# Optimization experiments

Hardware: AMD Instinct MI355X
Metric: run time of the kernel (lower is better)

Reference implementation:

```python
import jax, jax.numpy as jnp
import numpy as np

DECAY = 0.8
COMMITMENT_WEIGHT = 1.0
EPS = 1e-5


def setup_inputs() -> dict:
    key = jax.random.key(0)
    k1, k2, k3 = jax.random.split(key, 3)
    B, T, D, K = 16, 2048, 512, 8192
    x = jax.random.normal(k1, (B, T, D), dtype=jnp.float32)
    embed = jax.random.normal(k2, (D, K), dtype=jnp.float32)
    cluster_size = jnp.ones((K,), dtype=jnp.float32)
    embed_avg = jax.random.normal(k3, (D, K), dtype=jnp.float32)
    return {"x": x, "embed": embed, "cluster_size": cluster_size, "embed_avg": embed_avg}


def reference(x, embed, cluster_size, embed_avg):
    B, T, D = x.shape
    K = embed.shape[1]
    flat = x.reshape(-1, D)  # [N, D]

    # squared L2 distance to each code: ||f||^2 - 2 f.e + ||e||^2  -> [N, K]
    dist = (flat * flat).sum(-1, keepdims=True) \
        - 2.0 * (flat @ embed) \
        + (embed * embed).sum(0, keepdims=True)
    embed_ind = jnp.argmin(dist, axis=1)  # [N] (== argmax of -dist)

    quantize = jnp.take(embed.T, embed_ind, axis=0).reshape(B, T, D)

    # ---- EMA codebook statistics (training-mode buffer updates) ----
    onehot_sum = jnp.zeros((K,), dtype=flat.dtype).at[embed_ind].add(1.0)  # [K]
    # flat.T @ onehot == segment-sum of tokens per code, transposed -> [D, K]
    embed_sum = jax.ops.segment_sum(flat, embed_ind, num_segments=K).T
    new_cluster_size = cluster_size * DECAY + (1.0 - DECAY) * onehot_sum
    new_embed_avg = embed_avg * DECAY + (1.0 - DECAY) * embed_sum
    n = new_cluster_size.sum()
    cs = (new_cluster_size + EPS) / (n + K * EPS) * n
    new_embed = new_embed_avg / cs[None, :]
    # (random re-init of unused codes is omitted: non-deterministic side effect)

    commitment_loss = jnp.mean((jax.lax.stop_gradient(quantize) - x) ** 2) * COMMITMENT_WEIGHT
    quantize_st = x + jax.lax.stop_gradient(quantize - x)  # straight-through

    return (quantize_st, embed_ind.reshape(B, T), commitment_loss,
            new_embed, new_cluster_size, new_embed_avg)
```

## Files before the change

### kernel.cpp

```cpp
#include <hip/hip_runtime.h>

#define NTOK   32768
#define DDIM   512
#define KCODES 8192
#define DK     (DDIM * KCODES)
#define DECAYF 0.8f
#define EPSF   1e-5f

using short8 = __attribute__((ext_vector_type(8))) short;
using f32x4  = __attribute__((ext_vector_type(4))) float;

#define WS_ESUMT  0
#define WS_ONEHOT DK
#define WS_ENORM  (DK + 8192)
#define WS_SCAL   (DK + 16384)
#define WS_PART   (WS_SCAL + 64)
#define WS_EHI    (WS_PART + 2 * NTOK)
#define WS_ELO    (WS_EHI + DK / 2)

__device__ __forceinline__ unsigned short bf16rne(float f) {
  unsigned u = __float_as_uint(f);
  unsigned r = u + 0x7FFFu + ((u >> 16) & 1u);
  return (unsigned short)(r >> 16);
}

__device__ __forceinline__ void gload_lds16(const unsigned short* g, unsigned short* l) {
  __builtin_amdgcn_global_load_lds(
      (const __attribute__((address_space(1))) unsigned int*)g,
      (__attribute__((address_space(3))) unsigned int*)l, 16, 0, 0);
}

__global__ __launch_bounds__(256) void prep_kernel(
    const float* __restrict__ x, const float* __restrict__ embed,
    const float* __restrict__ cluster_size,
    unsigned short* __restrict__ xhi, unsigned short* __restrict__ xlo,
    unsigned short* __restrict__ ehi, unsigned short* __restrict__ elo,
    float* __restrict__ e_norm, float* __restrict__ esumT,
    float* __restrict__ onehot, float* __restrict__ scal,
    unsigned long long* __restrict__ partials) {
  __shared__ float tile[32][33];
  __shared__ float part[8][32];
  __shared__ float w[4];
  const int bid = blockIdx.x;
  const int tid = threadIdx.x;

  if (bid < 8192) {
    const size_t i = ((size_t)bid * 256 + tid) * 8;
    const float4 v0 = *(const float4*)&x[i];
    const float4 v1 = *(const float4*)&x[i + 4];
    const float v[8] = {v0.x, v0.y, v0.z, v0.w, v1.x, v1.y, v1.z, v1.w};
    unsigned short h[8], l[8];
#pragma unroll
    for (int j = 0; j < 8; ++j) {
      h[j] = bf16rne(v[j]);
      l[j] = bf16rne(v[j] - __uint_as_float((unsigned)h[j] << 16));
    }
    uint4 H, L;
    H.x = h[0] | ((unsigned)h[1] << 16); H.y = h[2] | ((unsigned)h[3] << 16);
    H.z = h[4] | ((unsigned)h[5] << 16); H.w = h[6] | ((unsigned)h[7] << 16);
    L.x = l[0] | ((unsigned)l[1] << 16); L.y = l[2] | ((unsigned)l[3] << 16);
    L.z = l[4] | ((unsigned)l[5] << 16); L.w = l[6] | ((unsigned)l[7] << 16);
    *(uint4*)&xhi[i] = H;
    *(uint4*)&xlo[i] = L;
  } else if (bid < 8192 + 256) {
    const int k0 = (bid - 8192) * 32;
    const int tx = tid & 31;
    const int ty = tid >> 5;
    float sq = 0.f;
#pragma unroll 1
    for (int d0 = 0; d0 < DDIM; d0 += 32) {
      __syncthreads();
#pragma unroll
      for (int j = 0; j < 4; ++j) {
        const int dl = ty + j * 8;
        const float v = embed[(size_t)(d0 + dl) * KCODES + k0 + tx];
        tile[dl][tx] = v;
        sq += v * v;
      }
      __syncthreads();
#pragma unroll
      for (int j = 0; j < 4; ++j) {
        const int kl = ty + j * 8;
        const size_t idx = (size_t)(k0 + kl) * DDIM + d0 + tx;
        const float v = tile[tx][kl];
        const unsigned short h = bf16rne(v);
        ehi[idx] = h;
        elo[idx] = bf16rne(v - __uint_as_float((unsigned)h << 16));
      }
    }
    part[ty][tx] = sq;
    __syncthreads();
    if (ty == 0) {
      float s = 0.f;
#pragma unroll
      for (int j = 0; j < 8; ++j) s += part[j][tx];
      e_norm[k0 + tx] = s;
    }
  } else if (bid < 8192 + 256 + 2048) {
    const int zb = bid - (8192 + 256);
    const size_t off = (size_t)zb * 2048 + (size_t)tid * 8;
    const float4 z = {0.f, 0.f, 0.f, 0.f};
    *(float4*)&esumT[off] = z;
    *(float4*)&esumT[off + 4] = z;
  } else {
    const int b = bid - (8192 + 256 + 2048);
    onehot[b * 256 + tid] = 0.f;
    const size_t pbase = (size_t)b * 1024 + (size_t)tid * 4;
    const ulonglong2 ff = {~0ull, ~0ull};
    *(ulonglong2*)&partials[pbase] = ff;
    *(ulonglong2*)&partials[pbase + 2] = ff;
    float s = cluster_size[b * 256 + tid];
#pragma unroll
    for (int off = 32; off > 0; off >>= 1) s += __shfl_down(s, off);
    if ((tid & 63) == 0) w[tid >> 6] = s;
    __syncthreads();
    if (tid == 0) {
      scal[2 + b] = w[0] + w[1] + w[2] + w[3];
      if (b == 0) { scal[0] = 0.f; scal[1] = 0.f; }
    }
  }
}

__global__ __launch_bounds__(256) void argmin_mfma_kernel(
    const unsigned short* __restrict__ xhi, const unsigned short* __restrict__ xlo,
    const unsigned short* __restrict__ ehi, const unsigned short* __restrict__ elo,
    const float* __restrict__ e_norm, unsigned long long* __restrict__ partials) {
  __shared__ unsigned short Ahs[128 * 32];
  __shared__ unsigned short Als[128 * 32];
  __shared__ unsigned short Bhs[128 * 32];
  __shared__ unsigned short Bls[128 * 32];

  const int t    = threadIdx.x;
  const int wid  = t >> 6;
  const int lid  = t & 63;
  const int kblk = blockIdx.x;
  const int tokbase = blockIdx.y * 128;
  const int kbase   = kblk * 128;

  const int wrow = wid >> 1, wcol = wid & 1;
  const int m16  = lid & 15, kq = lid >> 4;

  const int srow = lid >> 2;
  const int gcol = ((lid & 3) ^ ((srow >> 1) & 3)) * 8;
  const int fsw = (kq ^ ((m16 >> 1) & 3)) * 8;

  f32x4 acc[4][4];
#pragma unroll
  for (int i = 0; i < 4; ++i)
#pragma unroll
    for (int j = 0; j < 4; ++j) acc[i][j] = (f32x4)0.f;

  const unsigned short* Ahg = xhi + (size_t)tokbase * DDIM;
  const unsigned short* Alg = xlo + (size_t)tokbase * DDIM;
  const unsigned short* Bhg = ehi + (size_t)kbase * DDIM;
  const unsigned short* Blg = elo + (size_t)kbase * DDIM;

#pragma unroll 1
  for (int d0 = 0; d0 < DDIM; d0 += 32) {
    __syncthreads();
#pragma unroll
    for (int p = 0; p < 2; ++p) {
      const int chunk = wid + p * 4;
      const size_t go = (size_t)(chunk * 16 + srow) * DDIM + d0 + gcol;
      gload_lds16(Ahg + go, &Ahs[chunk * 512]);
      gload_lds16(Alg + go, &Als[chunk * 512]);
      gload_lds16(Bhg + go, &Bhs[chunk * 512]);
      gload_lds16(Blg + go, &Bls[chunk * 512]);
    }
    __syncthreads();
    short8 bh[4], bl[4];
#pragma unroll
    for (int j = 0; j < 4; ++j) {
      const int r = (wcol * 64 + j * 16 + m16) * 32 + fsw;
      bh[j] = *(const short8*)&Bhs[r];
      bl[j] = *(const short8*)&Bls[r];
    }
#pragma unroll
    for (int i = 0; i < 4; ++i) {
      const int r = (wrow * 64 + i * 16 + m16) * 32 + fsw;
      const short8 ah = *(const short8*)&Ahs[r];
      const short8 al = *(const short8*)&Als[r];
#pragma unroll
      for (int j = 0; j < 4; ++j) {
        acc[i][j] = __builtin_amdgcn_mfma_f32_16x16x32_bf16(ah, bh[j], acc[i][j], 0, 0, 0);
        acc[i][j] = __builtin_amdgcn_mfma_f32_16x16x32_bf16(ah, bl[j], acc[i][j], 0, 0, 0);
        acc[i][j] = __builtin_amdgcn_mfma_f32_16x16x32_bf16(al, bh[j], acc[i][j], 0, 0, 0);
      }
    }
  }

  float en[4];
#pragma unroll
  for (int j = 0; j < 4; ++j)
    en[j] = e_norm[kbase + wcol * 64 + j * 16 + m16];

  __syncthreads();
  unsigned long long* red = (unsigned long long*)Ahs;
#pragma unroll
  for (int i = 0; i < 4; ++i) {
#pragma unroll
    for (int r = 0; r < 4; ++r) {
      unsigned long long best = 0xFFFFFFFFFFFFFFFFull;
#pragma unroll
      for (int j = 0; j < 4; ++j) {
        const float s = en[j] - 2.0f * acc[i][j][r];
        unsigned u = __float_as_uint(s);
        u = (u & 0x80000000u) ? ~u : (u | 0x80000000u);
        const unsigned k = (unsigned)(kbase + wcol * 64 + j * 16 + m16);
        const unsigned long long c = ((unsigned long long)u << 32) | k;
        best = (c < best) ? c : best;
      }
#pragma unroll
      for (int s = 1; s < 16; s <<= 1) {
        const unsigned long long c = __shfl_xor(best, s);
        best = (c < best) ? c : best;
      }
      if (m16 == 0)
        red[(wrow * 64 + i * 16 + kq * 4 + r) * 2 + wcol] = best;
    }
  }
  __syncthreads();
  if (t < 128) {
    const unsigned long long a0 = red[t * 2], a1 = red[t * 2 + 1];
    const unsigned long long m = (a0 < a1) ? a0 : a1;
    atomicMin(&partials[tokbase + t], m);
  }
}

__global__ __launch_bounds__(256) void gather_stats_kernel(
    const float* __restrict__ x, const unsigned short* __restrict__ ehi,
    const unsigned short* __restrict__ elo,
    const unsigned long long* __restrict__ partials,
    float* __restrict__ quant_out, float* __restrict__ indf_out,
    float* __restrict__ embed_sumT, float* __restrict__ onehot,
    float* __restrict__ scal) {
  const int sub = threadIdx.x >> 7;
  const int t7  = threadIdx.x & 127;
  const int n   = blockIdx.x * 2 + sub;
  __shared__ int s_ind[2];
  __shared__ float wsum[4];
  if (t7 == 0) {
    const int k = (int)(partials[n] & 0xFFFFFFFFull);
    s_ind[sub] = k;
    indf_out[n] = (float)k;
    atomicAdd(&onehot[k], 1.0f);
  }
  __syncthreads();
  const int k = s_ind[sub];
  const int d4 = t7 * 4;
  const ushort4 h4 = *(const ushort4*)&ehi[(size_t)k * DDIM + d4];
  const ushort4 l4 = *(const ushort4*)&elo[(size_t)k * DDIM + d4];
  float4 e;
  e.x = __uint_as_float((unsigned)h4.x << 16) + __uint_as_float((unsigned)l4.x << 16);
  e.y = __uint_as_float((unsigned)h4.y << 16) + __uint_as_float((unsigned)l4.y << 16);
  e.z = __uint_as_float((unsigned)h4.z << 16) + __uint_as_float((unsigned)l4.z << 16);
  e.w = __uint_as_float((unsigned)h4.w << 16) + __uint_as_float((unsigned)l4.w << 16);
  const float4 xv = *(const float4*)&x[(size_t)n * DDIM + d4];
  *(float4*)&quant_out[(size_t)n * DDIM + d4] = e;
  atomicAdd(&embed_sumT[(size_t)k * DDIM + d4 + 0], xv.x);
  atomicAdd(&embed_sumT[(size_t)k * DDIM + d4 + 1], xv.y);
  atomicAdd(&embed_sumT[(size_t)k * DDIM + d4 + 2], xv.z);
  atomicAdd(&embed_sumT[(size_t)k * DDIM + d4 + 3], xv.w);
  const float dx0 = e.x - xv.x, dx1 = e.y - xv.y, dx2 = e.z - xv.z, dx3 = e.w - xv.w;
  float ls = dx0 * dx0 + dx1 * dx1 + dx2 * dx2 + dx3 * dx3;
#pragma unroll
  for (int off = 32; off > 0; off >>= 1) ls += __shfl_down(ls, off);
  if ((threadIdx.x & 63) == 0) wsum[threadIdx.x >> 6] = ls;
  __syncthreads();
  if (threadIdx.x == 0)
    atomicAdd(&scal[0], wsum[0] + wsum[1] + wsum[2] + wsum[3]);
}

__global__ __launch_bounds__(256) void finalize_kernel(
    const float* __restrict__ embed_avg, const float* __restrict__ embed_sumT,
    const float* __restrict__ cluster_size, const float* __restrict__ onehot,
    const float* __restrict__ scal,
    float* __restrict__ out_embed, float* __restrict__ out_avg,
    float* __restrict__ out_ncs, float* __restrict__ out_loss) {
  __shared__ float tile[32][33];
  __shared__ float sh_nsum;
  const int k0 = blockIdx.x * 32;
  const int d0 = blockIdx.y * 32;
  const int tx = threadIdx.x & 31;
  const int ty = threadIdx.x >> 5;
  if (threadIdx.x == 0) {
    float s = 0.f;
#pragma unroll
    for (int b = 0; b < 32; ++b) s += scal[2 + b];
    sh_nsum = DECAYF * s + (1.0f - DECAYF) * (float)NTOK;
  }
#pragma unroll
  for (int j = 0; j < 4; ++j) {
    const int kl = ty + j * 8;
    tile[kl][tx] = embed_sumT[(size_t)(k0 + kl) * DDIM + d0 + tx];
  }
  __syncthreads();
  const float nsum = sh_nsum;
  const float ncs = DECAYF * cluster_size[k0 + tx] + (1.0f - DECAYF) * onehot[k0 + tx];
  const float csv = (ncs + EPSF) / (nsum + (float)KCODES * EPSF) * nsum;
#pragma unroll
  for (int j = 0; j < 4; ++j) {
    const int dl = ty + j * 8;
    const size_t idx = (size_t)(d0 + dl) * KCODES + k0 + tx;
    const float nea = DECAYF * embed_avg[idx] + (1.0f - DECAYF) * tile[tx][dl];
    out_avg[idx] = nea;
    out_embed[idx] = nea / csv;
  }
  if (blockIdx.y == 0 && ty == 0)
    out_ncs[k0 + tx] = ncs;
  if (blockIdx.x == 0 && blockIdx.y == 0 && threadIdx.x == 0)
    out_loss[0] = scal[0] * (1.0f / ((float)NTOK * (float)DDIM));
}

extern "C" void kernel_launch(void* const* d_in, const int* in_sizes, int n_in,
                              void* d_out, int out_size, void* d_ws, size_t ws_size,
                              hipStream_t stream) {
  (void)in_sizes; (void)n_in; (void)out_size; (void)ws_size;
  const float* x            = (const float*)d_in[0];
  const float* embed        = (const float*)d_in[1];
  const float* cluster_size = (const float*)d_in[2];
  const float* embed_avg    = (const float*)d_in[3];

  float* out = (float*)d_out;
  float* out_quant = out;
  float* out_indf  = out + 16777216;
  float* out_loss  = out + 16777216 + 32768;
  float* out_embed = out + 16777216 + 32768 + 1;
  float* out_ncs   = out_embed + DK;
  float* out_avg   = out_ncs + KCODES;

  float* ws = (float*)d_ws;
  float* esumT  = ws + WS_ESUMT;
  float* onehot = ws + WS_ONEHOT;
  float* e_norm = ws + WS_ENORM;
  float* scal   = ws + WS_SCAL;
  unsigned long long* partials = (unsigned long long*)(ws + WS_PART);
  unsigned short* ehi = (unsigned short*)(ws + WS_EHI);
  unsigned short* elo = (unsigned short*)(ws + WS_ELO);

  unsigned short* xhi = (unsigned short*)d_out;
  unsigned short* xlo = xhi + (size_t)NTOK * DDIM;

  prep_kernel<<<8192 + 256 + 2048 + 32, 256, 0, stream>>>(
      x, embed, cluster_size, xhi, xlo, ehi, elo, e_norm, esumT, onehot, scal, partials);

  argmin_mfma_kernel<<<dim3(64, 256), 256, 0, stream>>>(
      xhi, xlo, ehi, elo, e_norm, partials);

  gather_stats_kernel<<<NTOK / 2, 256, 0, stream>>>(
      x, ehi, elo, partials, out_quant, out_indf, esumT, onehot, scal);

  finalize_kernel<<<dim3(KCODES / 32, DDIM / 32), 256, 0, stream>>>(
      embed_avg, esumT, cluster_size, onehot, scal,
      out_embed, out_avg, out_ncs, out_loss);
}
```

Measured before the change: 1.382 ms.

## Fuse four VQ kernels into one persistent cooperative kernel with grid syncs

Merges the prep, MFMA argmin, gather/stats and finalize kernels into one persistent cooperative kernel. Work items are distributed in grid-stride loops, and the phases are separated by grid.sync. This removes three kernel launches and the idle gaps between them. In exchange, the grid is capped at occupancy times 256 blocks, grid barriers are added, and the argmin block order changes, which may hurt cache reuse.

```diff
diff --git a/kernel.cpp b/kernel.cpp
--- a/kernel.cpp
+++ b/kernel.cpp
@@ -1,4 +1,7 @@
 #include <hip/hip_runtime.h>
+#include <hip/hip_cooperative_groups.h>
+
+namespace cg = cooperative_groups;
 
 #define NTOK   32768
 #define DDIM   512
@@ -18,6 +21,11 @@
 #define WS_EHI    (WS_PART + 2 * NTOK)
 #define WS_ELO    (WS_EHI + DK / 2)
 
+#define P_NBLK (8192 + 256 + 2048 + 32)
+#define G_NBLK (64 * 256)
+#define Q_NBLK (NTOK / 2)
+#define F_NBLK (256 * 16)
+
 __device__ __forceinline__ unsigned short bf16rne(float f) {
   unsigned u = __float_as_uint(f);
   unsigned r = u + 0x7FFFu + ((u >> 16) & 1u);
@@ -30,286 +38,290 @@
       (__attribute__((address_space(3))) unsigned int*)l, 16, 0, 0);
 }
 
-__global__ __launch_bounds__(256) void prep_kernel(
+__global__ __launch_bounds__(256, 3) void vq_fused_kernel(
     const float* __restrict__ x, const float* __restrict__ embed,
-    const float* __restrict__ cluster_size,
+    const float* __restrict__ cluster_size, const float* __restrict__ embed_avg,
+    float* __restrict__ out_quant, float* __restrict__ out_indf,
+    float* __restrict__ out_loss, float* __restrict__ out_embed,
+    float* __restrict__ out_ncs, float* __restrict__ out_avg,
     unsigned short* __restrict__ xhi, unsigned short* __restrict__ xlo,
     unsigned short* __restrict__ ehi, unsigned short* __restrict__ elo,
     float* __restrict__ e_norm, float* __restrict__ esumT,
     float* __restrict__ onehot, float* __restrict__ scal,
     unsigned long long* __restrict__ partials) {
-  __shared__ float tile[32][33];
-  __shared__ float part[8][32];
-  __shared__ float w[4];
-  const int bid = blockIdx.x;
+  __shared__ __align__(16) unsigned short sbuf[4 * 128 * 32];
+  cg::grid_group grid = cg::this_grid();
   const int tid = threadIdx.x;
-
-  if (bid < 8192) {
-    const size_t i = ((size_t)bid * 256 + tid) * 8;
-    const float4 v0 = *(const float4*)&x[i];
-    const float4 v1 = *(const float4*)&x[i + 4];
-    const float v[8] = {v0.x, v0.y, v0.z, v0.w, v1.x, v1.y, v1.z, v1.w};
-    unsigned short h[8], l[8];
-#pragma unroll
-    for (int j = 0; j < 8; ++j) {
-      h[j] = bf16rne(v[j]);
-      l[j] = bf16rne(v[j] - __uint_as_float((unsigned)h[j] << 16));
+  const int nb  = gridDim.x;
+
+  {
+    float* tile33 = (float*)sbuf;
+    float* part8  = tile33 + 32 * 33;
+    float* wred   = part8 + 8 * 32;
+    for (int bid = blockIdx.x; bid < P_NBLK; bid += nb) {
+      if (bid < 8192) {
+        const size_t i = ((size_t)bid * 256 + tid) * 8;
+        const float4 v0 = *(const float4*)&x[i];
+        const float4 v1 = *(const float4*)&x[i + 4];
+        const float v[8] = {v0.x, v0.y, v0.z, v0.w, v1.x, v1.y, v1.z, v1.w};
+        unsigned short h[8], l[8];
+#pragma unroll
+        for (int j = 0; j < 8; ++j) {
+          h[j] = bf16rne(v[j]);
+          l[j] = bf16rne(v[j] - __uint_as_float((unsigned)h[j] << 16));
+        }
+        uint4 H, L;
+        H.x = h[0] | ((unsigned)h[1] << 16); H.y = h[2] | ((unsigned)h[3] << 16);
+        H.z = h[4] | ((unsigned)h[5] << 16); H.w = h[6] | ((unsigned)h[7] << 16);
+        L.x = l[0] | ((unsigned)l[1] << 16); L.y = l[2] | ((unsigned)l[3] << 16);
+        L.z = l[4] | ((unsigned)l[5] << 16); L.w = l[6] | ((unsigned)l[7] << 16);
+        *(uint4*)&xhi[i] = H;
+        *(uint4*)&xlo[i] = L;
+      } else if (bid < 8192 + 256) {
+        const int k0 = (bid - 8192) * 32;
+        const int tx = tid & 31;
+        const int ty = tid >> 5;
+        float sq = 0.f;
+#pragma unroll 1
+        for (int d0 = 0; d0 < DDIM; d0 += 32) {
+          __syncthreads();
+#pragma unroll
+          for (int j = 0; j < 4; ++j) {
+            const int dl = ty + j * 8;
+            const float v = embed[(size_t)(d0 + dl) * KCODES + k0 + tx];
+            tile33[dl * 33 + tx] = v;
+            sq += v * v;
+          }
+          __syncthreads();
+#pragma unroll
+          for (int j = 0; j < 4; ++j) {
+            const int kl = ty + j * 8;
+            const size_t idx = (size_t)(k0 + kl) * DDIM + d0 + tx;
+            const float v = tile33[tx * 33 + kl];
+            const unsigned short h = bf16rne(v);
+            ehi[idx] = h;
+            elo[idx] = bf16rne(v - __uint_as_float((unsigned)h << 16));
+          }
+        }
+        part8[ty * 32 + tx] = sq;
+        __syncthreads();
+        if (ty == 0) {
+          float s = 0.f;
+#pragma unroll
+          for (int j = 0; j < 8; ++j) s += part8[j * 32 + tx];
+          e_norm[k0 + tx] = s;
+        }
+      } else if (bid < 8192 + 256 + 2048) {
+        const int zb = bid - (8192 + 256);
+        const size_t off = (size_t)zb * 2048 + (size_t)tid * 8;
+        const float4 z = {0.f, 0.f, 0.f, 0.f};
+        *(float4*)&esumT[off] = z;
+        *(float4*)&esumT[off + 4] = z;
+      } else {
+        const int b = bid - (8192 + 256 + 2048);
+        onehot[b * 256 + tid] = 0.f;
+        const size_t pbase = (size_t)b * 1024 + (size_t)tid * 4;
+        const ulonglong2 ff = {~0ull, ~0ull};
+        *(ulonglong2*)&partials[pbase] = ff;
+        *(ulonglong2*)&partials[pbase + 2] = ff;
+        float s = cluster_size[b * 256 + tid];
+#pragma unroll
+        for (int off = 32; off > 0; off >>= 1) s += __shfl_down(s, off);
+        if ((tid & 63) == 0) wred[tid >> 6] = s;
+        __syncthreads();
+        if (tid == 0) {
+          scal[2 + b] = wred[0] + wred[1] + wred[2] + wred[3];
+          if (b == 0) { scal[0] = 0.f; scal[1] = 0.f; }
+        }
+      }
+      __syncthreads();
     }
-    uint4 H, L;
-    H.x = h[0] | ((unsigned)h[1] << 16); H.y = h[2] | ((unsigned)h[3] << 16);
-    H.z = h[4] | ((unsigned)h[5] << 16); H.w = h[6] | ((unsigned)h[7] << 16);
-    L.x = l[0] | ((unsigned)l[1] << 16); L.y = l[2] | ((unsigned)l[3] << 16);
-    L.z = l[4] | ((unsigned)l[5] << 16); L.w = l[6] | ((unsigned)l[7] << 16);
-    *(uint4*)&xhi[i] = H;
-    *(uint4*)&xlo[i] = L;
-  } else if (bid < 8192 + 256) {
-    const int k0 = (bid - 8192) * 32;
+  }
+  __threadfence();
+  grid.sync();
+
+  {
+    unsigned short* Ahs = sbuf;
+    unsigned short* Als = sbuf + 4096;
+    unsigned short* Bhs = sbuf + 8192;
+    unsigned short* Bls = sbuf + 12288;
+
+    const int wid = tid >> 6;
+    const int lid = tid & 63;
+    const int wrow = wid >> 1, wcol = wid & 1;
+    const int m16 = lid & 15, kq = lid >> 4;
+    const int srow = lid >> 2;
+    const int gcol = ((lid & 3) ^ ((srow >> 1) & 3)) * 8;
+    const int fsw = (kq ^ ((m16 >> 1) & 3)) * 8;
+
+    for (int vb = blockIdx.x; vb < G_NBLK; vb += nb) {
+      const int kbase   = (vb & 63) * 128;
+      const int tokbase = (vb >> 6) * 128;
+
+      f32x4 acc[4][4];
+#pragma unroll
+      for (int i = 0; i < 4; ++i)
+#pragma unroll
+        for (int j = 0; j < 4; ++j) acc[i][j] = (f32x4)0.f;
+
+      const unsigned short* Ahg = xhi + (size_t)tokbase * DDIM;
+      const unsigned short* Alg = xlo + (size_t)tokbase * DDIM;
+      const unsigned short* Bhg = ehi + (size_t)kbase * DDIM;
+      const unsigned short* Blg = elo + (size_t)kbase * DDIM;
+
+#pragma unroll 1
+      for (int d0 = 0; d0 < DDIM; d0 += 32) {
+        __syncthreads();
+#pragma unroll
+        for (int p = 0; p < 2; ++p) {
+          const int chunk = wid + p * 4;
+          const size_t go = (size_t)(chunk * 16 + srow) * DDIM + d0 + gcol;
+          gload_lds16(Ahg + go, &Ahs[chunk * 512]);
+          gload_lds16(Alg + go, &Als[chunk * 512]);
+          gload_lds16(Bhg + go, &Bhs[chunk * 512]);
+          gload_lds16(Blg + go, &Bls[chunk * 512]);
+        }
+        __syncthreads();
+        short8 bh[4], bl[4];
+#pragma unroll
+        for (int j = 0; j < 4; ++j) {
+          const int r = (wcol * 64 + j * 16 + m16) * 32 + fsw;
+          bh[j] = *(const short8*)&Bhs[r];
+          bl[j] = *(const short8*)&Bls[r];
+        }
+#pragma unroll
+        for (int i = 0; i < 4; ++i) {
+          const int r = (wrow * 64 + i * 16 + m16) * 32 + fsw;
+          const short8 ah = *(const short8*)&Ahs[r];
+          const short8 al = *(const short8*)&Als[r];
+#pragma unroll
+          for (int j = 0; j < 4; ++j) {
+            acc[i][j] = __builtin_amdgcn_mfma_f32_16x16x32_bf16(ah, bh[j], acc[i][j], 0, 0, 0);
+            acc[i][j] = __builtin_amdgcn_mfma_f32_16x16x32_bf16(ah, bl[j], acc[i][j], 0, 0, 0);
+            acc[i][j] = __builtin_amdgcn_mfma_f32_16x16x32_bf16(al, bh[j], acc[i][j], 0, 0, 0);
+          }
+        }
+      }
+
+      float en[4];
+#pragma unroll
+      for (int j = 0; j < 4; ++j)
+        en[j] = e_norm[kbase + wcol * 64 + j * 16 + m16];
+
+      __syncthreads();
+      unsigned long long* red = (unsigned long long*)Ahs;
+#pragma unroll
+      for (int i = 0; i < 4; ++i) {
+#pragma unroll
+        for (int r = 0; r < 4; ++r) {
+          unsigned long long best = 0xFFFFFFFFFFFFFFFFull;
+#pragma unroll
+          for (int j = 0; j < 4; ++j) {
+            const float s = en[j] - 2.0f * acc[i][j][r];
+            unsigned u = __float_as_uint(s);
+            u = (u & 0x80000000u) ? ~u : (u | 0x80000000u);
+            const unsigned k = (unsigned)(kbase + wcol * 64 + j * 16 + m16);
+            const unsigned long long c = ((unsigned long long)u << 32) | k;
+            best = (c < best) ? c : best;
+          }
+#pragma unroll
+          for (int s = 1; s < 16; s <<= 1) {
+            const unsigned long long c = __shfl_xor(best, s);
+            best = (c < best) ? c : best;
+          }
+          if (m16 == 0)
+            red[(wrow * 64 + i * 16 + kq * 4 + r) * 2 + wcol] = best;
+        }
+      }
+      __syncthreads();
+      if (tid < 128) {
+        const unsigned long long a0 = red[tid * 2], a1 = red[tid * 2 + 1];
+        const unsigned long long m = (a0 < a1) ? a0 : a1;
+        atomicMin(&partials[tokbase + tid], m);
+      }
+      __syncthreads();
+    }
+  }
+  __threadfence();
+  grid.sync();
+
+  {
+    int*   s_ind = (int*)sbuf;
+    float* wsum  = ((float*)sbuf) + 2;
+    const int sub = tid >> 7;
+    const int t7  = tid & 127;
+    for (int vb = blockIdx.x; vb < Q_NBLK; vb += nb) {
+      const int n = vb * 2 + sub;
+      if (t7 == 0) {
+        const int k = (int)(partials[n] & 0xFFFFFFFFull);
+        s_ind[sub] = k;
+        out_indf[n] = (float)k;
+        atomicAdd(&onehot[k], 1.0f);
+      }
+      __syncthreads();
+      const int k = s_ind[sub];
+      const int d4 = t7 * 4;
+      const ushort4 h4 = *(const ushort4*)&ehi[(size_t)k * DDIM + d4];
+      const ushort4 l4 = *(const ushort4*)&elo[(size_t)k * DDIM + d4];
+      float4 e;
+      e.x = __uint_as_float((unsigned)h4.x << 16) + __uint_as_float((unsigned)l4.x << 16);
+      e.y = __uint_as_float((unsigned)h4.y << 16) + __uint_as_float((unsigned)l4.y << 16);
+      e.z = __uint_as_float((unsigned)h4.z << 16) + __uint_as_float((unsigned)l4.z << 16);
+      e.w = __uint_as_float((unsigned)h4.w << 16) + __uint_as_float((unsigned)l4.w << 16);
+      const float4 xv = *(const float4*)&x[(size_t)n * DDIM + d4];
+      *(float4*)&out_quant[(size_t)n * DDIM + d4] = e;
+      atomicAdd(&esumT[(size_t)k * DDIM + d4 + 0], xv.x);
+      atomicAdd(&esumT[(size_t)k * DDIM + d4 + 1], xv.y);
+      atomicAdd(&esumT[(size_t)k * DDIM + d4 + 2], xv.z);
+      atomicAdd(&esumT[(size_t)k * DDIM + d4 + 3], xv.w);
+      const float dx0 = e.x - xv.x, dx1 = e.y - xv.y, dx2 = e.z - xv.z, dx3 = e.w - xv.w;
+      float ls = dx0 * dx0 + dx1 * dx1 + dx2 * dx2 + dx3 * dx3;
+#pragma unroll
+      for (int off = 32; off > 0; off >>= 1) ls += __shfl_down(ls, off);
+      if ((tid & 63) == 0) wsum[tid >> 6] = ls;
+      __syncthreads();
+      if (tid == 0)
+        atomicAdd(&scal[0], wsum[0] + wsum[1] + wsum[2] + wsum[3]);
+      __syncthreads();
+    }
+  }
+  __threadfence();
+  grid.sync();
+
+  {
+    float* tile33 = (float*)sbuf;
+    float csum = 0.f;
+#pragma unroll
+    for (int b = 0; b < 32; ++b) csum += scal[2 + b];
+    const float nsum = DECAYF * csum + (1.0f - DECAYF) * (float)NTOK;
     const int tx = tid & 31;
     const int ty = tid >> 5;
-    float sq = 0.f;
-#pragma unroll 1
-    for (int d0 = 0; d0 < DDIM; d0 += 32) {
-      __syncthreads();
+    for (int vb = blockIdx.x; vb < F_NBLK; vb += nb) {
+      const int k0 = (vb & 255) * 32;
+      const int d0 = (vb >> 8) * 32;
+#pragma unroll
+      for (int j = 0; j < 4; ++j) {
+        const int kl = ty + j * 8;
+        tile33[kl * 33 + tx] = esumT[(size_t)(k0 + kl) * DDIM + d0 + tx];
+      }
+      __syncthreads();
+      const float ncs = DECAYF * cluster_size[k0 + tx] + (1.0f - DECAYF) * onehot[k0 + tx];
+      const float csv = (ncs + EPSF) / (nsum + (float)KCODES * EPSF) * nsum;
 #pragma unroll
       for (int j = 0; j < 4; ++j) {
         const int dl = ty + j * 8;
-        const float v = embed[(size_t)(d0 + dl) * KCODES + k0 + tx];
-        tile[dl][tx] = v;
-        sq += v * v;
-      }
-      __syncthreads();
-#pragma unroll
-      for (int j = 0; j < 4; ++j) {
-        const int kl = ty + j * 8;
-        const size_t idx = (size_t)(k0 + kl) * DDIM + d0 + tx;
-        const float v = tile[tx][kl];
-        const unsigned short h = bf16rne(v);
-        ehi[idx] = h;
-        elo[idx] = bf16rne(v - __uint_as_float((unsigned)h << 16));
-      }
+        const size_t idx = (size_t)(d0 + dl) * KCODES + k0 + tx;
+        const float nea = DECAYF * embed_avg[idx] + (1.0f - DECAYF) * tile33[tx * 33 + dl];
+        out_avg[idx] = nea;
+        out_embed[idx] = nea / csv;
+      }
+      if ((vb >> 8) == 0 && ty == 0)
+        out_ncs[k0 + tx] = ncs;
+      if (vb == 0 && tid == 0)
+        out_loss[0] = scal[0] * (1.0f / ((float)NTOK * (float)DDIM));
+      __syncthreads();
     }
-    part[ty][tx] = sq;
-    __syncthreads();
-    if (ty == 0) {
-      float s = 0.f;
-#pragma unroll
-      for (int j = 0; j < 8; ++j) s += part[j][tx];
-      e_norm[k0 + tx] = s;
-    }
-  } else if (bid < 8192 + 256 + 2048) {
-    const int zb = bid - (8192 + 256);
-    const size_t off = (size_t)zb * 2048 + (size_t)tid * 8;
-    const float4 z = {0.f, 0.f, 0.f, 0.f};
-    *(float4*)&esumT[off] = z;
-    *(float4*)&esumT[off + 4] = z;
-  } else {
-    const int b = bid - (8192 + 256 + 2048);
-    onehot[b * 256 + tid] = 0.f;
-    const size_t pbase = (size_t)b * 1024 + (size_t)tid * 4;
-    const ulonglong2 ff = {~0ull, ~0ull};
-    *(ulonglong2*)&partials[pbase] = ff;
-    *(ulonglong2*)&partials[pbase + 2] = ff;
-    float s = cluster_size[b * 256 + tid];
-#pragma unroll
-    for (int off = 32; off > 0; off >>= 1) s += __shfl_down(s, off);
-    if ((tid & 63) == 0) w[tid >> 6] = s;
-    __syncthreads();
-    if (tid == 0) {
-      scal[2 + b] = w[0] + w[1] + w[2] + w[3];
-      if (b == 0) { scal[0] = 0.f; scal[1] = 0.f; }
-    }
-  }
-}
-
-__global__ __launch_bounds__(256) void argmin_mfma_kernel(
-    const unsigned short* __restrict__ xhi, const unsigned short* __restrict__ xlo,
-    const unsigned short* __restrict__ ehi, const unsigned short* __restrict__ elo,
-    const float* __restrict__ e_norm, unsigned long long* __restrict__ partials) {
-  __shared__ unsigned short Ahs[128 * 32];
-  __shared__ unsigned short Als[128 * 32];
-  __shared__ unsigned short Bhs[128 * 32];
-  __shared__ unsigned short Bls[128 * 32];
-
-  const int t    = threadIdx.x;
-  const int wid  = t >> 6;
-  const int lid  = t & 63;
-  const int kblk = blockIdx.x;
-  const int tokbase = blockIdx.y * 128;
-  const int kbase   = kblk * 128;
-
-  const int wrow = wid >> 1, wcol = wid & 1;
-  const int m16  = lid & 15, kq = lid >> 4;
-
-  const int srow = lid >> 2;
-  const int gcol = ((lid & 3) ^ ((srow >> 1) & 3)) * 8;
-  const int fsw = (kq ^ ((m16 >> 1) & 3)) * 8;
-
-  f32x4 acc[4][4];
-#pragma unroll
-  for (int i = 0; i < 4; ++i)
-#pragma unroll
-    for (int j = 0; j < 4; ++j) acc[i][j] = (f32x4)0.f;
-
-  const unsigned short* Ahg = xhi + (size_t)tokbase * DDIM;
-  const unsigned short* Alg = xlo + (size_t)tokbase * DDIM;
-  const unsigned short* Bhg = ehi + (size_t)kbase * DDIM;
-  const unsigned short* Blg = elo + (size_t)kbase * DDIM;
-
-#pragma unroll 1
-  for (int d0 = 0; d0 < DDIM; d0 += 32) {
-    __syncthreads();
-#pragma unroll
-    for (int p = 0; p < 2; ++p) {
-      const int chunk = wid + p * 4;
-      const size_t go = (size_t)(chunk * 16 + srow) * DDIM + d0 + gcol;
-      gload_lds16(Ahg + go, &Ahs[chunk * 512]);
-      gload_lds16(Alg + go, &Als[chunk * 512]);
-      gload_lds16(Bhg + go, &Bhs[chunk * 512]);
-      gload_lds16(Blg + go, &Bls[chunk * 512]);
-    }
-    __syncthreads();
-    short8 bh[4], bl[4];
-#pragma unroll
-    for (int j = 0; j < 4; ++j) {
-      const int r = (wcol * 64 + j * 16 + m16) * 32 + fsw;
-      bh[j] = *(const short8*)&Bhs[r];
-      bl[j] = *(const short8*)&Bls[r];
-    }
-#pragma unroll
-    for (int i = 0; i < 4; ++i) {
-      const int r = (wrow * 64 + i * 16 + m16) * 32 + fsw;
-      const short8 ah = *(const short8*)&Ahs[r];
-      const short8 al = *(const short8*)&Als[r];
-#pragma unroll
-      for (int j = 0; j < 4; ++j) {
-        acc[i][j] = __builtin_amdgcn_mfma_f32_16x16x32_bf16(ah, bh[j], acc[i][j], 0, 0, 0);
-        acc[i][j] = __builtin_amdgcn_mfma_f32_16x16x32_bf16(ah, bl[j], acc[i][j], 0, 0, 0);
-        acc[i][j] = __builtin_amdgcn_mfma_f32_16x16x32_bf16(al, bh[j], acc[i][j], 0, 0, 0);
-      }
-    }
-  }
-
-  float en[4];
-#pragma unroll
-  for (int j = 0; j < 4; ++j)
-    en[j] = e_norm[kbase + wcol * 64 + j * 16 + m16];
-
-  __syncthreads();
-  unsigned long long* red = (unsigned long long*)Ahs;
-#pragma unroll
-  for (int i = 0; i < 4; ++i) {
-#pragma unroll
-    for (int r = 0; r < 4; ++r) {
-      unsigned long long best = 0xFFFFFFFFFFFFFFFFull;
-#pragma unroll
-      for (int j = 0; j < 4; ++j) {
-        const float s = en[j] - 2.0f * acc[i][j][r];
-        unsigned u = __float_as_uint(s);
-        u = (u & 0x80000000u) ? ~u : (u | 0x80000000u);
-        const unsigned k = (unsigned)(kbase + wcol * 64 + j * 16 + m16);
-        const unsigned long long c = ((unsigned long long)u << 32) | k;
-        best = (c < best) ? c : best;
-      }
-#pragma unroll
-      for (int s = 1; s < 16; s <<= 1) {
-        const unsigned long long c = __shfl_xor(best, s);
-        best = (c < best) ? c : best;
-      }
-      if (m16 == 0)
-        red[(wrow * 64 + i * 16 + kq * 4 + r) * 2 + wcol] = best;
-    }
-  }
-  __syncthreads();
-  if (t < 128) {
-    const unsigned long long a0 = red[t * 2], a1 = red[t * 2 + 1];
-    const unsigned long long m = (a0 < a1) ? a0 : a1;
-    atomicMin(&partials[tokbase + t], m);
-  }
-}
-
-__global__ __launch_bounds__(256) void gather_stats_kernel(
-    const float* __restrict__ x, const unsigned short* __restrict__ ehi,
-    const unsigned short* __restrict__ elo,
-    const unsigned long long* __restrict__ partials,
-    float* __restrict__ quant_out, float* __restrict__ indf_out,
-    float* __restrict__ embed_sumT, float* __restrict__ onehot,
-    float* __restrict__ scal) {
-  const int sub = threadIdx.x >> 7;
-  const int t7  = threadIdx.x & 127;
-  const int n   = blockIdx.x * 2 + sub;
-  __shared__ int s_ind[2];
-  __shared__ float wsum[4];
-  if (t7 == 0) {
-    const int k = (int)(partials[n] & 0xFFFFFFFFull);
-    s_ind[sub] = k;
-    indf_out[n] = (float)k;
-    atomicAdd(&onehot[k], 1.0f);
-  }
-  __syncthreads();
-  const int k = s_ind[sub];
-  const int d4 = t7 * 4;
-  const ushort4 h4 = *(const ushort4*)&ehi[(size_t)k * DDIM + d4];
-  const ushort4 l4 = *(const ushort4*)&elo[(size_t)k * DDIM + d4];
-  float4 e;
-  e.x = __uint_as_float((unsigned)h4.x << 16) + __uint_as_float((unsigned)l4.x << 16);
-  e.y = __uint_as_float((unsigned)h4.y << 16) + __uint_as_float((unsigned)l4.y << 16);
-  e.z = __uint_as_float((unsigned)h4.z << 16) + __uint_as_float((unsigned)l4.z << 16);
-  e.w = __uint_as_float((unsigned)h4.w << 16) + __uint_as_float((unsigned)l4.w << 16);
-  const float4 xv = *(const float4*)&x[(size_t)n * DDIM + d4];
-  *(float4*)&quant_out[(size_t)n * DDIM + d4] = e;
-  atomicAdd(&embed_sumT[(size_t)k * DDIM + d4 + 0], xv.x);
-  atomicAdd(&embed_sumT[(size_t)k * DDIM + d4 + 1], xv.y);
-  atomicAdd(&embed_sumT[(size_t)k * DDIM + d4 + 2], xv.z);
-  atomicAdd(&embed_sumT[(size_t)k * DDIM + d4 + 3], xv.w);
-  const float dx0 = e.x - xv.x, dx1 = e.y - xv.y, dx2 = e.z - xv.z, dx3 = e.w - xv.w;
-  float ls = dx0 * dx0 + dx1 * dx1 + dx2 * dx2 + dx3 * dx3;
-#pragma unroll
-  for (int off = 32; off > 0; off >>= 1) ls += __shfl_down(ls, off);
-  if ((threadIdx.x & 63) == 0) wsum[threadIdx.x >> 6] = ls;
-  __syncthreads();
-  if (threadIdx.x == 0)
-    atomicAdd(&scal[0], wsum[0] + wsum[1] + wsum[2] + wsum[3]);
-}
-
-__global__ __launch_bounds__(256) void finalize_kernel(
-    const float* __restrict__ embed_avg, const float* __restrict__ embed_sumT,
-    const float* __restrict__ cluster_size, const float* __restrict__ onehot,
-    const float* __restrict__ scal,
-    float* __restrict__ out_embed, float* __restrict__ out_avg,
-    float* __restrict__ out_ncs, float* __restrict__ out_loss) {
-  __shared__ float tile[32][33];
-  __shared__ float sh_nsum;
-  const int k0 = blockIdx.x * 32;
-  const int d0 = blockIdx.y * 32;
-  const int tx = threadIdx.x & 31;
-  const int ty = threadIdx.x >> 5;
-  if (threadIdx.x == 0) {
-    float s = 0.f;
-#pragma unroll
-    for (int b = 0; b < 32; ++b) s += scal[2 + b];
-    sh_nsum = DECAYF * s + (1.0f - DECAYF) * (float)NTOK;
-  }
-#pragma unroll
-  for (int j = 0; j < 4; ++j) {
-    const int kl = ty + j * 8;
-    tile[kl][tx] = embed_sumT[(size_t)(k0 + kl) * DDIM + d0 + tx];
-  }
-  __syncthreads();
-  const float nsum = sh_nsum;
-  const float ncs = DECAYF * cluster_size[k0 + tx] + (1.0f - DECAYF) * onehot[k0 + tx];
-  const float csv = (ncs + EPSF) / (nsum + (float)KCODES * EPSF) * nsum;
-#pragma unroll
-  for (int j = 0; j < 4; ++j) {
-    const int dl = ty + j * 8;
-    const size_t idx = (size_t)(d0 + dl) * KCODES + k0 + tx;
-    const float nea = DECAYF * embed_avg[idx] + (1.0f - DECAYF) * tile[tx][dl];
-    out_avg[idx] = nea;
-    out_embed[idx] = nea / csv;
-  }
-  if (blockIdx.y == 0 && ty == 0)
-    out_ncs[k0 + tx] = ncs;
-  if (blockIdx.x == 0 && blockIdx.y == 0 && threadIdx.x == 0)
-    out_loss[0] = scal[0] * (1.0f / ((float)NTOK * (float)DDIM));
+  }
 }
 
 extern "C" void kernel_launch(void* const* d_in, const int* in_sizes, int n_in,
@@ -341,16 +353,23 @@
   unsigned short* xhi = (unsigned short*)d_out;
   unsigned short* xlo = xhi + (size_t)NTOK * DDIM;
 
-  prep_kernel<<<8192 + 256 + 2048 + 32, 256, 0, stream>>>(
-      x, embed, cluster_size, xhi, xlo, ehi, elo, e_norm, esumT, onehot, scal, partials);
-
-  argmin_mfma_kernel<<<dim3(64, 256), 256, 0, stream>>>(
-      xhi, xlo, ehi, elo, e_norm, partials);
-
-  gather_stats_kernel<<<NTOK / 2, 256, 0, stream>>>(
-      x, ehi, elo, partials, out_quant, out_indf, esumT, onehot, scal);
-
-  finalize_kernel<<<dim3(KCODES / 32, DDIM / 32), 256, 0, stream>>>(
-      embed_avg, esumT, cluster_size, onehot, scal,
-      out_embed, out_avg, out_ncs, out_loss);
+  static int perCU = -1;
+  if (perCU < 0) {
+    if (hipOccupancyMaxActiveBlocksPerMultiprocessor(&perCU, vq_fused_kernel, 256, 0)
+            != hipSuccess || perCU < 1)
+      perCU = 2;
+  }
+  int grid = perCU * 256;
+  if (grid > 1280) grid = 1280;
+
+  void* args[] = {
+      (void*)&x, (void*)&embed, (void*)&cluster_size, (void*)&embed_avg,
+      (void*)&out_quant, (void*)&out_indf, (void*)&out_loss, (void*)&out_embed,
+      (void*)&out_ncs, (void*)&out_avg,
+      (void*)&xhi, (void*)&xlo, (void*)&ehi, (void*)&elo,
+      (void*)&e_norm, (void*)&esumT, (void*)&onehot, (void*)&scal,
+      (void*)&partials};
+
+  hipLaunchCooperativeKernel((const void*)vq_fused_kernel, dim3(grid), dim3(256),
+                             args, 0, stream);
 }
```

Measured after the change: 2.077 ms. 50.3% more time.

## Rewrite argmin GEMM as 256x256 double-buffered, 8-wave pipelined MFMA kernel

Applied to the files above, without the earlier changes.

The distance GEMM kernel moves from a 128x128 tile with 4 waves and a single LDS buffer to a 256x256 tile with 8 waves, split into four quadrant phases. It double-buffers LDS with explicit vmcnt waits and s_setprio around the MFMA phases, so global-to-LDS loads overlap compute. The three-term bf16 split (hi*hi, hi*lo, lo*hi) becomes 24 K-steps over hi/lo slices instead of inline triple MFMAs. This targets load latency and barrier stalls and raises reuse per loaded byte. The cost is larger register and LDS pressure (launch bounds of 512 threads, 2 blocks) and fragile hand-tuned waitcnt scheduling.

```diff
diff --git a/kernel.cpp b/kernel.cpp
--- a/kernel.cpp
+++ b/kernel.cpp
@@ -29,6 +29,11 @@
       (const __attribute__((address_space(1))) unsigned int*)g,
       (__attribute__((address_space(3))) unsigned int*)l, 16, 0, 0);
 }
+
+#define BAR() do { __builtin_amdgcn_sched_barrier(0); \
+  __builtin_amdgcn_s_barrier(); __builtin_amdgcn_sched_barrier(0); } while (0)
+#define VMCNT6() asm volatile("s_waitcnt vmcnt(6)" ::: "memory")
+#define VMCNT8() asm volatile("s_waitcnt vmcnt(8)" ::: "memory")
 
 __global__ __launch_bounds__(256) void prep_kernel(
     const float* __restrict__ x, const float* __restrict__ embed,
@@ -121,109 +126,164 @@
   }
 }
 
-__global__ __launch_bounds__(256) void argmin_mfma_kernel(
+#define PHASE_MFMA(Q) do {                                                  \
+  __builtin_amdgcn_s_setprio(1);                                            \
+  _Pragma("unroll") for (int fm_ = 0; fm_ < 4; ++fm_)                       \
+  _Pragma("unroll") for (int fn_ = 0; fn_ < 2; ++fn_)                       \
+  _Pragma("unroll") for (int ks_ = 0; ks_ < 2; ++ks_)                       \
+    acc[Q][fm_][fn_] = __builtin_amdgcn_mfma_f32_16x16x32_bf16(             \
+        Areg[fm_][ks_], Breg[fn_][ks_], acc[Q][fm_][fn_], 0, 0, 0);         \
+  __builtin_amdgcn_s_setprio(0);                                            \
+} while (0)
+
+__global__ __launch_bounds__(512, 2) void argmin_mfma_kernel(
     const unsigned short* __restrict__ xhi, const unsigned short* __restrict__ xlo,
     const unsigned short* __restrict__ ehi, const unsigned short* __restrict__ elo,
     const float* __restrict__ e_norm, unsigned long long* __restrict__ partials) {
-  __shared__ unsigned short Ahs[128 * 32];
-  __shared__ unsigned short Als[128 * 32];
-  __shared__ unsigned short Bhs[128 * 32];
-  __shared__ unsigned short Bls[128 * 32];
-
-  const int t    = threadIdx.x;
-  const int wid  = t >> 6;
-  const int lid  = t & 63;
-  const int kblk = blockIdx.x;
-  const int tokbase = blockIdx.y * 128;
-  const int kbase   = kblk * 128;
-
-  const int wrow = wid >> 1, wcol = wid & 1;
-  const int m16  = lid & 15, kq = lid >> 4;
-
-  const int srow = lid >> 2;
-  const int gcol = ((lid & 3) ^ ((srow >> 1) & 3)) * 8;
-  const int fsw = (kq ^ ((m16 >> 1) & 3)) * 8;
-
-  f32x4 acc[4][4];
-#pragma unroll
-  for (int i = 0; i < 4; ++i)
-#pragma unroll
-    for (int j = 0; j < 4; ++j) acc[i][j] = (f32x4)0.f;
-
-  const unsigned short* Ahg = xhi + (size_t)tokbase * DDIM;
-  const unsigned short* Alg = xlo + (size_t)tokbase * DDIM;
-  const unsigned short* Bhg = ehi + (size_t)kbase * DDIM;
-  const unsigned short* Blg = elo + (size_t)kbase * DDIM;
+  __shared__ unsigned short sA[2][2][128 * 64];
+  __shared__ unsigned short sB[2][2][128 * 64];
+
+  const int tid = threadIdx.x;
+  const int wid = tid >> 6;
+  const int lid = tid & 63;
+  const int wr  = wid >> 2;
+  const int wc  = wid & 3;
+  const int m16 = lid & 15, kq = lid >> 4;
+  const int kbase   = blockIdx.x * 256;
+  const int tokbase = blockIdx.y * 256;
+
+  const int w2q0 = wid * 2, w2q1 = w2q0 + 1;
+  const int l8 = lid >> 3, g8 = lid & 7;
+  const size_t sgo0 = (size_t)(w2q0 * 8 + l8) * DDIM + (size_t)((g8 ^ l8) * 8);
+  const size_t sgo1 = (size_t)(w2q1 * 8 + l8) * DDIM + (size_t)((g8 ^ l8) * 8);
+
+  f32x4 acc[4][4][2];
+#pragma unroll
+  for (int q = 0; q < 4; ++q)
+#pragma unroll
+    for (int i = 0; i < 4; ++i)
+#pragma unroll
+      for (int j = 0; j < 2; ++j) acc[q][i][j] = (f32x4)0.f;
+
+  short8 Areg[4][2];
+  short8 Breg[2][2];
+
+  auto stageA = [&](int h, int kt, int bf) {
+    const int ktc = kt < 24 ? kt : 23;
+    const unsigned short* sp = (ktc < 16 ? xhi : xlo)
+        + (size_t)(tokbase + h * 128) * DDIM + ((ktc & 7) << 6);
+    gload_lds16(sp + sgo0, &sA[bf][h][w2q0 * 512]);
+    gload_lds16(sp + sgo1, &sA[bf][h][w2q1 * 512]);
+  };
+  auto stageB = [&](int h, int kt, int bf) {
+    const int ktc = kt < 24 ? kt : 23;
+    const unsigned short* sp = ((ktc >= 8 && ktc < 16) ? elo : ehi)
+        + (size_t)(kbase + h * 128) * DDIM + ((ktc & 7) << 6);
+    gload_lds16(sp + sgo0, &sB[bf][h][w2q0 * 512]);
+    gload_lds16(sp + sgo1, &sB[bf][h][w2q1 * 512]);
+  };
+  auto loadA = [&](int bf, int mh) {
+#pragma unroll
+    for (int fm = 0; fm < 4; ++fm)
+#pragma unroll
+      for (int ks = 0; ks < 2; ++ks) {
+        const int r = wr * 64 + fm * 16 + m16;
+        const int grp = (ks * 4 + kq) ^ (m16 & 7);
+        Areg[fm][ks] = *(const short8*)&sA[bf][mh][r * 64 + grp * 8];
+      }
+  };
+  auto loadB = [&](int bf, int nh) {
+#pragma unroll
+    for (int fn = 0; fn < 2; ++fn)
+#pragma unroll
+      for (int ks = 0; ks < 2; ++ks) {
+        const int r = wc * 32 + fn * 16 + m16;
+        const int grp = (ks * 4 + kq) ^ (m16 & 7);
+        Breg[fn][ks] = *(const short8*)&sB[bf][nh][r * 64 + grp * 8];
+      }
+  };
+
+  stageA(0, 0, 0); stageB(0, 0, 0); stageA(1, 0, 0); stageB(1, 0, 0);
+  stageB(0, 1, 1); stageA(1, 1, 1);
+  VMCNT6();
+  BAR();
 
 #pragma unroll 1
-  for (int d0 = 0; d0 < DDIM; d0 += 32) {
-    __syncthreads();
-#pragma unroll
-    for (int p = 0; p < 2; ++p) {
-      const int chunk = wid + p * 4;
-      const size_t go = (size_t)(chunk * 16 + srow) * DDIM + d0 + gcol;
-      gload_lds16(Ahg + go, &Ahs[chunk * 512]);
-      gload_lds16(Alg + go, &Als[chunk * 512]);
-      gload_lds16(Bhg + go, &Bhs[chunk * 512]);
-      gload_lds16(Blg + go, &Bls[chunk * 512]);
-    }
-    __syncthreads();
-    short8 bh[4], bl[4];
-#pragma unroll
-    for (int j = 0; j < 4; ++j) {
-      const int r = (wcol * 64 + j * 16 + m16) * 32 + fsw;
-      bh[j] = *(const short8*)&Bhs[r];
-      bl[j] = *(const short8*)&Bls[r];
-    }
-#pragma unroll
-    for (int i = 0; i < 4; ++i) {
-      const int r = (wrow * 64 + i * 16 + m16) * 32 + fsw;
-      const short8 ah = *(const short8*)&Ahs[r];
-      const short8 al = *(const short8*)&Als[r];
-#pragma unroll
-      for (int j = 0; j < 4; ++j) {
-        acc[i][j] = __builtin_amdgcn_mfma_f32_16x16x32_bf16(ah, bh[j], acc[i][j], 0, 0, 0);
-        acc[i][j] = __builtin_amdgcn_mfma_f32_16x16x32_bf16(ah, bl[j], acc[i][j], 0, 0, 0);
-        acc[i][j] = __builtin_amdgcn_mfma_f32_16x16x32_bf16(al, bh[j], acc[i][j], 0, 0, 0);
+  for (int s = 0; s < 24; ++s) {
+    const int cur = s & 1, nxt = cur ^ 1;
+    loadA(cur, 0); loadB(cur, 0);
+    stageA(0, s + 1, nxt);
+    BAR();
+    PHASE_MFMA(0);
+    BAR();
+    loadA(cur, 1);
+    stageB(1, s + 1, nxt);
+    BAR();
+    PHASE_MFMA(1);
+    VMCNT8();
+    BAR();
+    loadB(cur, 1);
+    stageB(0, s + 2, cur);
+    BAR();
+    PHASE_MFMA(2);
+    BAR();
+    loadA(cur, 0);
+    stageA(1, s + 2, cur);
+    BAR();
+    PHASE_MFMA(3);
+    VMCNT6();
+    BAR();
+  }
+
+  asm volatile("s_waitcnt vmcnt(0)" ::: "memory");
+  __syncthreads();
+
+  float en[2][2];
+#pragma unroll
+  for (int nh = 0; nh < 2; ++nh)
+#pragma unroll
+    for (int fn = 0; fn < 2; ++fn)
+      en[nh][fn] = e_norm[kbase + nh * 128 + wc * 32 + fn * 16 + m16];
+
+  unsigned long long* red = (unsigned long long*)&sA[0][0][0];
+  const int mh_arr[4] = {0, 1, 1, 0};
+  const int nh_arr[4] = {0, 0, 1, 1};
+#pragma unroll
+  for (int q = 0; q < 4; ++q) {
+    const int mh = mh_arr[q], nh = nh_arr[q];
+#pragma unroll
+    for (int fm = 0; fm < 4; ++fm) {
+#pragma unroll
+      for (int r = 0; r < 4; ++r) {
+        unsigned long long best = 0xFFFFFFFFFFFFFFFFull;
+#pragma unroll
+        for (int fn = 0; fn < 2; ++fn) {
+          const float sc = en[nh][fn] - 2.0f * acc[q][fm][fn][r];
+          unsigned u = __float_as_uint(sc);
+          u = (u & 0x80000000u) ? ~u : (u | 0x80000000u);
+          const unsigned k = (unsigned)(kbase + nh * 128 + wc * 32 + fn * 16 + m16);
+          const unsigned long long c = ((unsigned long long)u << 32) | k;
+          best = (c < best) ? c : best;
+        }
+#pragma unroll
+        for (int sh = 1; sh < 16; sh <<= 1) {
+          const unsigned long long c = __shfl_xor(best, sh);
+          best = (c < best) ? c : best;
+        }
+        if (m16 == 0)
+          red[(mh * 128 + wr * 64 + fm * 16 + kq * 4 + r) * 8 + nh * 4 + wc] = best;
       }
     }
   }
-
-  float en[4];
-#pragma unroll
-  for (int j = 0; j < 4; ++j)
-    en[j] = e_norm[kbase + wcol * 64 + j * 16 + m16];
-
   __syncthreads();
-  unsigned long long* red = (unsigned long long*)Ahs;
-#pragma unroll
-  for (int i = 0; i < 4; ++i) {
-#pragma unroll
-    for (int r = 0; r < 4; ++r) {
-      unsigned long long best = 0xFFFFFFFFFFFFFFFFull;
-#pragma unroll
-      for (int j = 0; j < 4; ++j) {
-        const float s = en[j] - 2.0f * acc[i][j][r];
-        unsigned u = __float_as_uint(s);
-        u = (u & 0x80000000u) ? ~u : (u | 0x80000000u);
-        const unsigned k = (unsigned)(kbase + wcol * 64 + j * 16 + m16);
-        const unsigned long long c = ((unsigned long long)u << 32) | k;
-        best = (c < best) ? c : best;
-      }
-#pragma unroll
-      for (int s = 1; s < 16; s <<= 1) {
-        const unsigned long long c = __shfl_xor(best, s);
-        best = (c < best) ? c : best;
-      }
-      if (m16 == 0)
-        red[(wrow * 64 + i * 16 + kq * 4 + r) * 2 + wcol] = best;
-    }
-  }
-  __syncthreads();
-  if (t < 128) {
-    const unsigned long long a0 = red[t * 2], a1 = red[t * 2 + 1];
-    const unsigned long long m = (a0 < a1) ? a0 : a1;
-    atomicMin(&partials[tokbase + t], m);
+  if (tid < 256) {
+    unsigned long long m = red[tid * 8];
+#pragma unroll
+    for (int c = 1; c < 8; ++c) {
+      const unsigned long long v = red[tid * 8 + c];
+      m = (v < m) ? v : m;
+    }
+    atomicMin(&partials[tokbase + tid], m);
   }
 }
 
@@ -344,7 +404,7 @@
   prep_kernel<<<8192 + 256 + 2048 + 32, 256, 0, stream>>>(
       x, embed, cluster_size, xhi, xlo, ehi, elo, e_norm, esumT, onehot, scal, partials);
 
-  argmin_mfma_kernel<<<dim3(64, 256), 256, 0, stream>>>(
+  argmin_mfma_kernel<<<dim3(KCODES / 256, NTOK / 256), 512, 0, stream>>>(
       xhi, xlo, ehi, elo, e_norm, partials);
 
   gather_stats_kernel<<<NTOK / 2, 256, 0, stream>>>(
```

Result: slower. 1.506 ms (+8.9%).
